# Optimization experiments

Measured on AMD Instinct MI355X. Metric: run time of the kernel, lower is better.

Reference implementation:

```python
import jax, jax.numpy as jnp
import numpy as np

B, C, H, W = 16, 256, 32, 32
AD, SC, R = 16, 32, 4


def _conv1x1(x, w, b):
    # x: [B,Cin,H,W], w: [Cout,Cin], b: [Cout]
    return jnp.einsum('oc,bchw->bohw', w, x) + b[None, :, None, None]


def setup_inputs() -> dict:
    key = jax.random.key(0)
    ks = jax.random.split(key, 12)
    p = lambda k, shape: (jax.random.normal(k, shape, dtype=jnp.float32) * 0.02)
    return {
        'x': jax.random.normal(ks[0], (B, C, H, W), dtype=jnp.float32),
        'fc1_w': p(ks[1], (C // R, C)), 'fc1_b': jnp.zeros((C // R,), jnp.float32),
        'fc2_w': p(ks[2], (C, C // R)), 'fc2_b': jnp.zeros((C,), jnp.float32),
        'qkv_w': p(ks[3], (AD * 2 + SC, SC)), 'qkv_b': jnp.zeros((AD * 2 + SC,), jnp.float32),
        'proj_w': p(ks[4], (SC, SC)), 'proj_b': jnp.zeros((SC,), jnp.float32),
        'ffn1_w': p(ks[5], (4 * C, C)), 'ffn1_b': jnp.zeros((4 * C,), jnp.float32),
        'ffn2_w': p(ks[6], (C, 4 * C)), 'ffn2_b': jnp.zeros((C,), jnp.float32),
    }


def reference(x, fc1_w, fc1_b, fc2_w, fc2_b, qkv_w, qkv_b, proj_w, proj_b,
              ffn1_w, ffn1_b, ffn2_w, ffn2_b):
    # --- DynamicChannelSelect: SE gate then channel split ---
    s = x.mean(axis=(2, 3), keepdims=True)                       # [B,C,1,1]
    s = jax.nn.relu(_conv1x1(s, fc1_w, fc1_b))
    s = jax.nn.sigmoid(_conv1x1(s, fc2_w, fc2_b))
    xg = x * s
    attn_part, non_attn_part = xg[:, :SC], xg[:, SC:]

    # --- SHSA: single-head self-attention on SC channels ---
    qkv = _conv1x1(attn_part, qkv_w, qkv_b)                      # [B,2*AD+SC,H,W]
    q = qkv[:, :AD].reshape(B, AD, H * W)
    k = qkv[:, AD:2 * AD].reshape(B, AD, H * W)
    v = qkv[:, 2 * AD:].reshape(B, SC, H * W)
    scale = AD ** -0.5
    attn = jax.nn.softmax(jnp.einsum('bcn,bcm->bnm', q, k) * scale, axis=-1)  # [B,N,N]
    out = jnp.einsum('bcm,bnm->bcn', v, attn).reshape(B, SC, H, W)
    attn_out = _conv1x1(out, proj_w, proj_b)

    # --- concat + 1x1-conv FFN ---
    y = jnp.concatenate([attn_out, non_attn_part], axis=1)       # [B,C,H,W]
    h = jax.nn.relu(_conv1x1(y, ffn1_w, ffn1_b))                 # [B,4C,H,W]
    return _conv1x1(h, ffn2_w, ffn2_b)                           # [B,C,H,W]
```

## Files before the change

kernel.cpp:

```cpp
#include <hip/hip_runtime.h>
#include <cstdint>
#include <cstddef>

#define BB 16
#define CC 256
#define NP 1024

typedef __attribute__((ext_vector_type(8))) short bf16x8;
typedef __attribute__((ext_vector_type(4))) float f32x4;
typedef unsigned short u16;

__device__ __forceinline__ u16 f2bf(float f) {
    union { float f; uint32_t u; } v; v.f = f;
    uint32_t u = v.u;
    return (u16)((u + 0x7FFFu + ((u >> 16) & 1u)) >> 16);
}

__global__ __launch_bounds__(256)
void se_mean_kernel(const float* __restrict__ x, float* __restrict__ s_mean) {
    int bc = blockIdx.x;
    const float* p = x + (size_t)bc * NP;
    int t = threadIdx.x;
    float4 v = *(const float4*)(p + t * 4);
    float s = (v.x + v.y) + (v.z + v.w);
#pragma unroll
    for (int off = 32; off; off >>= 1) s += __shfl_down(s, off, 64);
    __shared__ float red[4];
    if ((t & 63) == 0) red[t >> 6] = s;
    __syncthreads();
    if (t == 0) s_mean[bc] = (red[0] + red[1] + red[2] + red[3]) * (1.0f / NP);
}

__global__ __launch_bounds__(256)
void se_mlp_kernel(const float* __restrict__ s_mean,
                   const float* __restrict__ fc1_w, const float* __restrict__ fc1_b,
                   const float* __restrict__ fc2_w, const float* __restrict__ fc2_b,
                   float* __restrict__ sig) {
    int b = blockIdx.x;
    __shared__ float sm[CC];
    __shared__ float h1[64];
    int t = threadIdx.x;
    sm[t] = s_mean[b * CC + t];
    __syncthreads();
    if (t < 64) {
        float a = fc1_b[t];
        for (int c = 0; c < CC; ++c) a += fc1_w[t * CC + c] * sm[c];
        h1[t] = fmaxf(a, 0.f);
    }
    __syncthreads();
    float a = fc2_b[t];
#pragma unroll 8
    for (int c = 0; c < 64; ++c) a += fc2_w[t * 64 + c] * h1[c];
    sig[b * CC + t] = 1.f / (1.f + __expf(-a));
}

__global__ __launch_bounds__(256)
void scale_transpose_kernel(const float* __restrict__ x, const float* __restrict__ sig,
                            float* __restrict__ yg32, u16* __restrict__ ygt) {
    int nt = blockIdx.x, ct = blockIdx.y, b = blockIdx.z;
    __shared__ float tile[64][65];
    int t = threadIdx.x;
    const float* Xb = x + ((size_t)b * CC + ct * 64) * NP + nt * 64;
    float* ygb = yg32 + (size_t)b * 32 * NP + nt * 64;
#pragma unroll
    for (int p = 0; p < 4; ++p) {
        int e = t + p * 256;
        int c = e >> 4, n4 = (e & 15) * 4;
        float4 v = *(const float4*)&Xb[(size_t)c * NP + n4];
        float sc = sig[b * CC + ct * 64 + c];
        v.x *= sc; v.y *= sc; v.z *= sc; v.w *= sc;
        tile[c][n4] = v.x; tile[c][n4 + 1] = v.y; tile[c][n4 + 2] = v.z; tile[c][n4 + 3] = v.w;
        if (ct == 0 && c < 32) *(float4*)&ygb[(size_t)c * NP + n4] = v;
    }
    __syncthreads();
    u16* Yb = ygt + ((size_t)b * NP + nt * 64) * CC + ct * 64;
#pragma unroll
    for (int p = 0; p < 4; ++p) {
        int e = t + p * 256;
        int n = e >> 4, c4 = (e & 15) * 4;
        if (ct * 64 + c4 >= 32) {
            ushort4 o;
            o.x = f2bf(tile[c4][n]);     o.y = f2bf(tile[c4 + 1][n]);
            o.z = f2bf(tile[c4 + 2][n]); o.w = f2bf(tile[c4 + 3][n]);
            *(ushort4*)&Yb[(size_t)n * CC + c4] = o;
        }
    }
}

__global__ __launch_bounds__(256)
void qkv_kernel(const float* __restrict__ yg32,
                const float* __restrict__ W, const float* __restrict__ bias,
                u16* __restrict__ Qt, u16* __restrict__ Kt, u16* __restrict__ Vb) {
    int nt = blockIdx.x, b = blockIdx.y;
    const float* Xb = yg32 + (size_t)b * 32 * NP + nt * 64;
    __shared__ __align__(16) float xs[32][64];
    __shared__ float ws[64 * 32];
    __shared__ float bs[64];
    __shared__ float vtile[32][64];
    int t = threadIdx.x;
    for (int e = t * 4; e < 32 * 64; e += 1024) {
        int c = e >> 6, nn = e & 63;
        *(float4*)&xs[c][nn] = *(const float4*)&Xb[(size_t)c * NP + nn];
    }
    for (int e = t; e < 2048; e += 256) ws[e] = W[e];
    if (t < 64) bs[t] = bias[t];
    __syncthreads();
    int nn = t & 63, g = t >> 6;
    int n = nt * 64 + nn;
    float acc[16];
#pragma unroll
    for (int oc = 0; oc < 16; ++oc) {
        int o = g * 16 + oc;
        float a = bs[o];
#pragma unroll
        for (int c = 0; c < 32; ++c) a += ws[o * 32 + c] * xs[c][nn];
        acc[oc] = a;
    }
    if (g == 0) {
        u16* qr = Qt + ((size_t)b * NP + n) * 32;
        ushort4 z4; z4.x = 0; z4.y = 0; z4.z = 0; z4.w = 0;
#pragma unroll
        for (int j = 0; j < 16; j += 4) {
            ushort4 o4;
            o4.x = f2bf(acc[j] * 0.25f);     o4.y = f2bf(acc[j + 1] * 0.25f);
            o4.z = f2bf(acc[j + 2] * 0.25f); o4.w = f2bf(acc[j + 3] * 0.25f);
            *(ushort4*)&qr[j] = o4;
        }
        *(ushort4*)&qr[16] = z4; *(ushort4*)&qr[20] = z4;
        *(ushort4*)&qr[24] = z4; *(ushort4*)&qr[28] = z4;
    } else if (g == 1) {
        u16* kr = Kt + ((size_t)b * NP + n) * 32;
        ushort4 z4; z4.x = 0; z4.y = 0; z4.z = 0; z4.w = 0;
#pragma unroll
        for (int j = 0; j < 16; j += 4) {
            ushort4 k4;
            k4.x = f2bf(acc[j]);     k4.y = f2bf(acc[j + 1]);
            k4.z = f2bf(acc[j + 2]); k4.w = f2bf(acc[j + 3]);
            *(ushort4*)&kr[j] = k4;
        }
        *(ushort4*)&kr[16] = z4; *(ushort4*)&kr[20] = z4;
        *(ushort4*)&kr[24] = z4; *(ushort4*)&kr[28] = z4;
    } else {
#pragma unroll
        for (int oc = 0; oc < 16; ++oc) vtile[(g - 2) * 16 + oc][nn] = acc[oc];
    }
    __syncthreads();
    for (int e = t; e < 32 * 64; e += 256) {
        int c = e >> 6, nn2 = e & 63;
        Vb[(size_t)b * 32 * NP + (size_t)c * NP + nt * 64 + nn2] = f2bf(vtile[c][nn2]);
    }
}

__global__ __launch_bounds__(256)
void attn_mfma_kernel(const u16* __restrict__ Qt, const u16* __restrict__ Kt,
                      const u16* __restrict__ Vb,
                      const float* __restrict__ proj_w, const float* __restrict__ proj_b,
                      u16* __restrict__ ygt) {
    int b = blockIdx.x >> 4;
    int n0 = (blockIdx.x & 15) * 64;
    __shared__ __align__(16) u16 P_lds[4][16][40];
    __shared__ float al_lds[4][16];
    __shared__ float lv_lds[4][16];
    __shared__ float O_lds[4][16][33];
    __shared__ float pw_s[32][32];
    __shared__ float pb_s[32];
    int t = threadIdx.x;
    int w = t >> 6, lane = t & 63;
    int q = lane >> 4, idx = lane & 15;

    for (int e = t; e < 1024; e += 256) pw_s[e >> 5][e & 31] = proj_w[e];
    if (t < 32) pb_s[t] = proj_b[t];
    __syncthreads();

    const u16* Qb = Qt + (size_t)b * NP * 32;
    const u16* Kb = Kt + (size_t)b * NP * 32;
    const u16* Vp = Vb + (size_t)b * 32 * NP;

    int nrow = n0 + w * 16 + idx;
    bf16x8 aq = *(const bf16x8*)&Qb[(size_t)nrow * 32 + q * 8];

    f32x4 O0 = {0.f, 0.f, 0.f, 0.f}, O1 = {0.f, 0.f, 0.f, 0.f};
    float m_run[4] = {-1e30f, -1e30f, -1e30f, -1e30f};
    float l_run[4] = {0.f, 0.f, 0.f, 0.f};

    for (int m0 = 0; m0 < NP; m0 += 32) {
        bf16x8 bk0 = *(const bf16x8*)&Kb[(size_t)(m0 + idx) * 32 + q * 8];
        bf16x8 bk1 = *(const bf16x8*)&Kb[(size_t)(m0 + 16 + idx) * 32 + q * 8];
        bf16x8 va0 = *(const bf16x8*)&Vp[(size_t)idx * NP + m0 + q * 8];
        bf16x8 va1 = *(const bf16x8*)&Vp[(size_t)(16 + idx) * NP + m0 + q * 8];
        f32x4 z = {0.f, 0.f, 0.f, 0.f};
        f32x4 S0 = __builtin_amdgcn_mfma_f32_16x16x32_bf16(aq, bk0, z, 0, 0, 0);
        f32x4 S1 = __builtin_amdgcn_mfma_f32_16x16x32_bf16(aq, bk1, z, 0, 0, 0);
        float mx[4], p0[4], p1[4], alpha[4];
#pragma unroll
        for (int r = 0; r < 4; ++r) mx[r] = fmaxf(S0[r], S1[r]);
#pragma unroll
        for (int off = 1; off < 16; off <<= 1)
#pragma unroll
            for (int r = 0; r < 4; ++r) mx[r] = fmaxf(mx[r], __shfl_xor(mx[r], off, 64));
#pragma unroll
        for (int r = 0; r < 4; ++r) {
            float nm = fmaxf(m_run[r], mx[r]);
            alpha[r] = __expf(m_run[r] - nm);
            m_run[r] = nm;
            p0[r] = __expf(S0[r] - nm);
            p1[r] = __expf(S1[r] - nm);
        }
#pragma unroll
        for (int r = 0; r < 4; ++r) {
            float s = p0[r] + p1[r];
#pragma unroll
            for (int off = 1; off < 16; off <<= 1) s += __shfl_xor(s, off, 64);
            l_run[r] = l_run[r] * alpha[r] + s;
        }
#pragma unroll
        for (int r = 0; r < 4; ++r) {
            P_lds[w][q * 4 + r][idx]      = f2bf(p0[r]);
            P_lds[w][q * 4 + r][idx + 16] = f2bf(p1[r]);
        }
        if (idx == 0) {
#pragma unroll
            for (int r = 0; r < 4; ++r) al_lds[w][q * 4 + r] = alpha[r];
        }
        float an = al_lds[w][idx];
#pragma unroll
        for (int r = 0; r < 4; ++r) { O0[r] *= an; O1[r] *= an; }
        bf16x8 pf = *(const bf16x8*)&P_lds[w][idx][q * 8];
        O0 = __builtin_amdgcn_mfma_f32_16x16x32_bf16(va0, pf, O0, 0, 0, 0);
        O1 = __builtin_amdgcn_mfma_f32_16x16x32_bf16(va1, pf, O1, 0, 0, 0);
    }
    if (idx == 0) {
#pragma unroll
        for (int r = 0; r < 4; ++r) lv_lds[w][q * 4 + r] = l_run[r];
    }
    float linv = 1.0f / lv_lds[w][idx];
#pragma unroll
    for (int r = 0; r < 4; ++r) {
        O_lds[w][idx][q * 4 + r]      = O0[r] * linv;
        O_lds[w][idx][q * 4 + r + 16] = O1[r] * linv;
    }
    float o0[4], o1[4];
#pragma unroll
    for (int r = 0; r < 4; ++r) { o0[r] = pb_s[q * 4 + r]; o1[r] = pb_s[q * 4 + r + 16]; }
#pragma unroll
    for (int c = 0; c < 32; ++c) {
        float xv = O_lds[w][idx][c];
#pragma unroll
        for (int r = 0; r < 4; ++r) {
            o0[r] += pw_s[q * 4 + r][c] * xv;
            o1[r] += pw_s[q * 4 + r + 16][c] * xv;
        }
    }
    u16* yrow = ygt + ((size_t)b * NP + nrow) * CC;
    ushort4 w0, w1;
    w0.x = f2bf(o0[0]); w0.y = f2bf(o0[1]); w0.z = f2bf(o0[2]); w0.w = f2bf(o0[3]);
    w1.x = f2bf(o1[0]); w1.y = f2bf(o1[1]); w1.z = f2bf(o1[2]); w1.w = f2bf(o1[3]);
    *(ushort4*)&yrow[q * 4] = w0;
    *(ushort4*)&yrow[q * 4 + 16] = w1;
}

__global__ __launch_bounds__(256)
void convert_w_kernel(const float* __restrict__ w1, u16* __restrict__ d1,
                      const float* __restrict__ w2, u16* __restrict__ d2) {
    int blk = blockIdx.x;
    const float* src = (blk < 256) ? w1 : w2;
    u16* dst = (blk < 256) ? d1 : d2;
    int i = ((blk & 255) * 256 + threadIdx.x) * 4;
    float4 v = *(const float4*)(src + i);
    ushort4 o;
    o.x = f2bf(v.x); o.y = f2bf(v.y); o.z = f2bf(v.z); o.w = f2bf(v.w);
    *(ushort4*)(dst + i) = o;
}

template <int K, bool RELU, bool TRANS_OUT>
__global__ __launch_bounds__(256)
void mfma_gemm_kernel(const u16* __restrict__ A, const u16* __restrict__ Bt,
                      const float* __restrict__ bias, void* __restrict__ Yv, int M) {
    __shared__ __align__(16) u16 As[128][64];
    __shared__ __align__(16) u16 Bs[128][64];
    int mt = blockIdx.x, nt = blockIdx.y;
    const u16* Ab = A + (size_t)mt * 128 * K;
    const u16* Bb = Bt + (size_t)nt * 128 * K;
    int t = threadIdx.x;
    int w = t >> 6, lane = t & 63;
    int q = lane >> 4, idx = lane & 15;
    int wr = (w >> 1) * 64, wc = (w & 1) * 64;
    int srow = lane >> 3;
    int gch = (lane & 7) ^ srow;

    f32x4 acc[4][4];
#pragma unroll
    for (int i = 0; i < 4; ++i)
#pragma unroll
        for (int j = 0; j < 4; ++j) { f32x4 z = {0.f, 0.f, 0.f, 0.f}; acc[i][j] = z; }

    for (int k0 = 0; k0 < K; k0 += 64) {
        __syncthreads();
#pragma unroll
        for (int p = 0; p < 4; ++p) {
            int r = w * 32 + p * 8 + srow;
            __builtin_amdgcn_global_load_lds(
                (const __attribute__((address_space(1))) void*)(Ab + (size_t)r * K + k0 + gch * 8),
                (__attribute__((address_space(3))) void*)(&As[w * 32 + p * 8][0]),
                16, 0, 0);
        }
#pragma unroll
        for (int p = 0; p < 4; ++p) {
            int r = w * 32 + p * 8 + srow;
            __builtin_amdgcn_global_load_lds(
                (const __attribute__((address_space(1))) void*)(Bb + (size_t)r * K + k0 + gch * 8),
                (__attribute__((address_space(3))) void*)(&Bs[w * 32 + p * 8][0]),
                16, 0, 0);
        }
        __syncthreads();
#pragma unroll
        for (int h = 0; h < 2; ++h) {
            bf16x8 af[4], bfr[4];
#pragma unroll
            for (int i = 0; i < 4; ++i)
                af[i] = *(const bf16x8*)&As[wr + i * 16 + idx][(((q + 4 * h) ^ (idx & 7)) * 8)];
#pragma unroll
            for (int j = 0; j < 4; ++j)
                bfr[j] = *(const bf16x8*)&Bs[wc + j * 16 + idx][(((q + 4 * h) ^ (idx & 7)) * 8)];
#pragma unroll
            for (int i = 0; i < 4; ++i)
#pragma unroll
                for (int j = 0; j < 4; ++j)
                    acc[i][j] = __builtin_amdgcn_mfma_f32_16x16x32_bf16(af[i], bfr[j], acc[i][j], 0, 0, 0);
        }
    }

    if (TRANS_OUT) {
        u16* Y = (u16*)Yv;
#pragma unroll
        for (int i = 0; i < 4; ++i) {
            int m0 = mt * 128 + wr + i * 16 + q * 4;
            float b0 = bias[m0], b1 = bias[m0 + 1], b2 = bias[m0 + 2], b3 = bias[m0 + 3];
#pragma unroll
            for (int j = 0; j < 4; ++j) {
                int n = nt * 128 + wc + j * 16 + idx;
                f32x4 v = acc[i][j];
                float r0 = v.x + b0, r1 = v.y + b1, r2 = v.z + b2, r3 = v.w + b3;
                if (RELU) {
                    r0 = fmaxf(r0, 0.f); r1 = fmaxf(r1, 0.f);
                    r2 = fmaxf(r2, 0.f); r3 = fmaxf(r3, 0.f);
                }
                ushort4 o;
                o.x = f2bf(r0); o.y = f2bf(r1); o.z = f2bf(r2); o.w = f2bf(r3);
                *(ushort4*)&Y[(size_t)n * (size_t)M + m0] = o;
            }
        }
    } else {
        float* Y = (float*)Yv;
#pragma unroll
        for (int i = 0; i < 4; ++i) {
            int m0 = mt * 128 + wr + i * 16 + q * 4;
            float b0 = bias[m0], b1 = bias[m0 + 1], b2 = bias[m0 + 2], b3 = bias[m0 + 3];
#pragma unroll
            for (int j = 0; j < 4; ++j) {
                int ng = nt * 128 + wc + j * 16 + idx;
                int bb = ng >> 10, nn = ng & 1023;
                f32x4 v = acc[i][j];
                float* p = Y + ((size_t)bb * M + m0) * NP + nn;
                p[0]      = v.x + b0;
                p[NP]     = v.y + b1;
                p[2 * NP] = v.z + b2;
                p[3 * NP] = v.w + b3;
            }
        }
    }
}

extern "C" void kernel_launch(void* const* d_in, const int* in_sizes, int n_in,
                              void* d_out, int out_size, void* d_ws, size_t ws_size,
                              hipStream_t stream) {
    const float* x      = (const float*)d_in[0];
    const float* fc1_w  = (const float*)d_in[1];
    const float* fc1_b  = (const float*)d_in[2];
    const float* fc2_w  = (const float*)d_in[3];
    const float* fc2_b  = (const float*)d_in[4];
    const float* qkv_w  = (const float*)d_in[5];
    const float* qkv_b  = (const float*)d_in[6];
    const float* proj_w = (const float*)d_in[7];
    const float* proj_b = (const float*)d_in[8];
    const float* ffn1_w = (const float*)d_in[9];
    const float* ffn1_b = (const float*)d_in[10];
    const float* ffn2_w = (const float*)d_in[11];
    const float* ffn2_b = (const float*)d_in[12];
    float* out = (float*)d_out;

    u16* w1b = (u16*)d_ws;
    u16* w2b = w1b + 262144;
    u16* ygt = w2b + 262144;
    u16* ht  = ygt + (size_t)BB * NP * CC;
    float* sig  = (float*)ht;
    float* s_mean = sig + BB * CC;
    float* yg32 = s_mean + BB * CC;
    u16* Qt = (u16*)(yg32 + (size_t)BB * 32 * NP);
    u16* Kt = Qt + (size_t)BB * NP * 32;
    u16* Vb = Kt + (size_t)BB * NP * 32;

    se_mean_kernel<<<BB * CC, 256, 0, stream>>>(x, s_mean);
    convert_w_kernel<<<512, 256, 0, stream>>>(ffn1_w, w1b, ffn2_w, w2b);
    se_mlp_kernel<<<BB, 256, 0, stream>>>(s_mean, fc1_w, fc1_b, fc2_w, fc2_b, sig);
    scale_transpose_kernel<<<dim3(16, 4, BB), 256, 0, stream>>>(x, sig, yg32, ygt);
    qkv_kernel<<<dim3(16, BB), 256, 0, stream>>>(yg32, qkv_w, qkv_b, Qt, Kt, Vb);
    attn_mfma_kernel<<<BB * 16, 256, 0, stream>>>(Qt, Kt, Vb, proj_w, proj_b, ygt);

    mfma_gemm_kernel<256, true, true><<<dim3(8, 128), 256, 0, stream>>>(
        w1b, ygt, ffn1_b, (void*)ht, 1024);
    mfma_gemm_kernel<1024, false, false><<<dim3(2, 128), 256, 0, stream>>>(
        w2b, ht, ffn2_b, (void*)out, 256);
}
```

Before: 192.6 us.

## Fuse QKV into scale-transpose, split attention keys across waves, double-buffer GEMM

Folds the QKV 1x1 conv into the scale/transpose kernel using the already-scaled tile in shared memory, removing the fp32 staging buffer and one launch. The attention kernel now uses 512 threads, with two wave groups each covering half the keys and merging their softmax statistics in shared memory, to raise parallelism. The FFN GEMM double-buffers its LDS tiles so the next K-slice load overlaps the current MFMA work. The trade-offs are more shared memory per block and an extra merge step in attention.

Measured after the change: 181.7 us. 5.6% less time.

```diff
diff --git a/kernel.cpp b/kernel.cpp
--- a/kernel.cpp
+++ b/kernel.cpp
@@ -55,13 +55,21 @@
 }
 
 __global__ __launch_bounds__(256)
-void scale_transpose_kernel(const float* __restrict__ x, const float* __restrict__ sig,
-                            float* __restrict__ yg32, u16* __restrict__ ygt) {
+void scale_transpose_qkv_kernel(const float* __restrict__ x, const float* __restrict__ sig,
+                                const float* __restrict__ qW, const float* __restrict__ qB,
+                                u16* __restrict__ ygt, u16* __restrict__ Qt,
+                                u16* __restrict__ Kt, u16* __restrict__ Vb) {
     int nt = blockIdx.x, ct = blockIdx.y, b = blockIdx.z;
     __shared__ float tile[64][65];
+    __shared__ float ws[64 * 32];
+    __shared__ float bs[64];
+    __shared__ float vtile[32][64];
     int t = threadIdx.x;
     const float* Xb = x + ((size_t)b * CC + ct * 64) * NP + nt * 64;
-    float* ygb = yg32 + (size_t)b * 32 * NP + nt * 64;
+    if (ct == 0) {
+        for (int e = t; e < 2048; e += 256) ws[e] = qW[e];
+        if (t < 64) bs[t] = qB[t];
+    }
 #pragma unroll
     for (int p = 0; p < 4; ++p) {
         int e = t + p * 256;
@@ -70,7 +78,6 @@
         float sc = sig[b * CC + ct * 64 + c];
         v.x *= sc; v.y *= sc; v.z *= sc; v.w *= sc;
         tile[c][n4] = v.x; tile[c][n4 + 1] = v.y; tile[c][n4 + 2] = v.z; tile[c][n4 + 3] = v.w;
-        if (ct == 0 && c < 32) *(float4*)&ygb[(size_t)c * NP + n4] = v;
     }
     __syncthreads();
     u16* Yb = ygt + ((size_t)b * NP + nt * 64) * CC + ct * 64;
@@ -85,90 +92,74 @@
             *(ushort4*)&Yb[(size_t)n * CC + c4] = o;
         }
     }
-}
-
-__global__ __launch_bounds__(256)
-void qkv_kernel(const float* __restrict__ yg32,
-                const float* __restrict__ W, const float* __restrict__ bias,
-                u16* __restrict__ Qt, u16* __restrict__ Kt, u16* __restrict__ Vb) {
-    int nt = blockIdx.x, b = blockIdx.y;
-    const float* Xb = yg32 + (size_t)b * 32 * NP + nt * 64;
-    __shared__ __align__(16) float xs[32][64];
-    __shared__ float ws[64 * 32];
-    __shared__ float bs[64];
-    __shared__ float vtile[32][64];
-    int t = threadIdx.x;
-    for (int e = t * 4; e < 32 * 64; e += 1024) {
-        int c = e >> 6, nn = e & 63;
-        *(float4*)&xs[c][nn] = *(const float4*)&Xb[(size_t)c * NP + nn];
-    }
-    for (int e = t; e < 2048; e += 256) ws[e] = W[e];
-    if (t < 64) bs[t] = bias[t];
-    __syncthreads();
-    int nn = t & 63, g = t >> 6;
-    int n = nt * 64 + nn;
-    float acc[16];
-#pragma unroll
-    for (int oc = 0; oc < 16; ++oc) {
-        int o = g * 16 + oc;
-        float a = bs[o];
-#pragma unroll
-        for (int c = 0; c < 32; ++c) a += ws[o * 32 + c] * xs[c][nn];
-        acc[oc] = a;
-    }
-    if (g == 0) {
-        u16* qr = Qt + ((size_t)b * NP + n) * 32;
-        ushort4 z4; z4.x = 0; z4.y = 0; z4.z = 0; z4.w = 0;
-#pragma unroll
-        for (int j = 0; j < 16; j += 4) {
-            ushort4 o4;
-            o4.x = f2bf(acc[j] * 0.25f);     o4.y = f2bf(acc[j + 1] * 0.25f);
-            o4.z = f2bf(acc[j + 2] * 0.25f); o4.w = f2bf(acc[j + 3] * 0.25f);
-            *(ushort4*)&qr[j] = o4;
-        }
-        *(ushort4*)&qr[16] = z4; *(ushort4*)&qr[20] = z4;
-        *(ushort4*)&qr[24] = z4; *(ushort4*)&qr[28] = z4;
-    } else if (g == 1) {
-        u16* kr = Kt + ((size_t)b * NP + n) * 32;
-        ushort4 z4; z4.x = 0; z4.y = 0; z4.z = 0; z4.w = 0;
-#pragma unroll
-        for (int j = 0; j < 16; j += 4) {
-            ushort4 k4;
-            k4.x = f2bf(acc[j]);     k4.y = f2bf(acc[j + 1]);
-            k4.z = f2bf(acc[j + 2]); k4.w = f2bf(acc[j + 3]);
-            *(ushort4*)&kr[j] = k4;
-        }
-        *(ushort4*)&kr[16] = z4; *(ushort4*)&kr[20] = z4;
-        *(ushort4*)&kr[24] = z4; *(ushort4*)&kr[28] = z4;
-    } else {
-#pragma unroll
-        for (int oc = 0; oc < 16; ++oc) vtile[(g - 2) * 16 + oc][nn] = acc[oc];
-    }
-    __syncthreads();
-    for (int e = t; e < 32 * 64; e += 256) {
-        int c = e >> 6, nn2 = e & 63;
-        Vb[(size_t)b * 32 * NP + (size_t)c * NP + nt * 64 + nn2] = f2bf(vtile[c][nn2]);
-    }
-}
-
-__global__ __launch_bounds__(256)
+    if (ct == 0) {
+        int nn = t & 63, g = t >> 6;
+        int n = nt * 64 + nn;
+        float acc[16];
+#pragma unroll
+        for (int oc = 0; oc < 16; ++oc) {
+            int o = g * 16 + oc;
+            float a = bs[o];
+#pragma unroll
+            for (int c = 0; c < 32; ++c) a += ws[o * 32 + c] * tile[c][nn];
+            acc[oc] = a;
+        }
+        if (g == 0) {
+            u16* qr = Qt + ((size_t)b * NP + n) * 32;
+            ushort4 z4; z4.x = 0; z4.y = 0; z4.z = 0; z4.w = 0;
+#pragma unroll
+            for (int j = 0; j < 16; j += 4) {
+                ushort4 o4;
+                o4.x = f2bf(acc[j] * 0.25f);     o4.y = f2bf(acc[j + 1] * 0.25f);
+                o4.z = f2bf(acc[j + 2] * 0.25f); o4.w = f2bf(acc[j + 3] * 0.25f);
+                *(ushort4*)&qr[j] = o4;
+            }
+            *(ushort4*)&qr[16] = z4; *(ushort4*)&qr[20] = z4;
+            *(ushort4*)&qr[24] = z4; *(ushort4*)&qr[28] = z4;
+        } else if (g == 1) {
+            u16* kr = Kt + ((size_t)b * NP + n) * 32;
+            ushort4 z4; z4.x = 0; z4.y = 0; z4.z = 0; z4.w = 0;
+#pragma unroll
+            for (int j = 0; j < 16; j += 4) {
+                ushort4 k4;
+                k4.x = f2bf(acc[j]);     k4.y = f2bf(acc[j + 1]);
+                k4.z = f2bf(acc[j + 2]); k4.w = f2bf(acc[j + 3]);
+                *(ushort4*)&kr[j] = k4;
+            }
+            *(ushort4*)&kr[16] = z4; *(ushort4*)&kr[20] = z4;
+            *(ushort4*)&kr[24] = z4; *(ushort4*)&kr[28] = z4;
+        } else {
+#pragma unroll
+            for (int oc = 0; oc < 16; ++oc) vtile[(g - 2) * 16 + oc][nn] = acc[oc];
+        }
+        __syncthreads();
+        for (int e = t; e < 2048; e += 256) {
+            int c = e >> 6, nn2 = e & 63;
+            Vb[(size_t)b * 32 * NP + (size_t)c * NP + nt * 64 + nn2] = f2bf(vtile[c][nn2]);
+        }
+    }
+}
+
+__global__ __launch_bounds__(512)
 void attn_mfma_kernel(const u16* __restrict__ Qt, const u16* __restrict__ Kt,
                       const u16* __restrict__ Vb,
                       const float* __restrict__ proj_w, const float* __restrict__ proj_b,
                       u16* __restrict__ ygt) {
     int b = blockIdx.x >> 4;
     int n0 = (blockIdx.x & 15) * 64;
-    __shared__ __align__(16) u16 P_lds[4][16][40];
-    __shared__ float al_lds[4][16];
-    __shared__ float lv_lds[4][16];
-    __shared__ float O_lds[4][16][33];
+    __shared__ __align__(16) u16 P_lds[8][16][40];
+    __shared__ float al_lds[8][16];
+    __shared__ float sm_lds[8][16];
+    __shared__ float sl_lds[8][16];
+    __shared__ float O_lds[8][16][33];
     __shared__ float pw_s[32][32];
     __shared__ float pb_s[32];
     int t = threadIdx.x;
     int w = t >> 6, lane = t & 63;
     int q = lane >> 4, idx = lane & 15;
-
-    for (int e = t; e < 1024; e += 256) pw_s[e >> 5][e & 31] = proj_w[e];
+    int rg = w & 3, kh = w >> 2;
+
+    for (int e = t; e < 1024; e += 512) pw_s[e >> 5][e & 31] = proj_w[e];
     if (t < 32) pb_s[t] = proj_b[t];
     __syncthreads();
 
@@ -176,14 +167,15 @@
     const u16* Kb = Kt + (size_t)b * NP * 32;
     const u16* Vp = Vb + (size_t)b * 32 * NP;
 
-    int nrow = n0 + w * 16 + idx;
+    int nrow = n0 + rg * 16 + idx;
     bf16x8 aq = *(const bf16x8*)&Qb[(size_t)nrow * 32 + q * 8];
 
     f32x4 O0 = {0.f, 0.f, 0.f, 0.f}, O1 = {0.f, 0.f, 0.f, 0.f};
     float m_run[4] = {-1e30f, -1e30f, -1e30f, -1e30f};
     float l_run[4] = {0.f, 0.f, 0.f, 0.f};
 
-    for (int m0 = 0; m0 < NP; m0 += 32) {
+    int mbase = kh * 512;
+    for (int m0 = mbase; m0 < mbase + 512; m0 += 32) {
         bf16x8 bk0 = *(const bf16x8*)&Kb[(size_t)(m0 + idx) * 32 + q * 8];
         bf16x8 bk1 = *(const bf16x8*)&Kb[(size_t)(m0 + 16 + idx) * 32 + q * 8];
         bf16x8 va0 = *(const bf16x8*)&Vp[(size_t)idx * NP + m0 + q * 8];
@@ -231,32 +223,48 @@
     }
     if (idx == 0) {
 #pragma unroll
-        for (int r = 0; r < 4; ++r) lv_lds[w][q * 4 + r] = l_run[r];
-    }
-    float linv = 1.0f / lv_lds[w][idx];
+        for (int r = 0; r < 4; ++r) {
+            sm_lds[w][q * 4 + r] = m_run[r];
+            sl_lds[w][q * 4 + r] = l_run[r];
+        }
+    }
 #pragma unroll
     for (int r = 0; r < 4; ++r) {
-        O_lds[w][idx][q * 4 + r]      = O0[r] * linv;
-        O_lds[w][idx][q * 4 + r + 16] = O1[r] * linv;
-    }
-    float o0[4], o1[4];
-#pragma unroll
-    for (int r = 0; r < 4; ++r) { o0[r] = pb_s[q * 4 + r]; o1[r] = pb_s[q * 4 + r + 16]; }
-#pragma unroll
-    for (int c = 0; c < 32; ++c) {
-        float xv = O_lds[w][idx][c];
+        O_lds[w][idx][q * 4 + r]      = O0[r];
+        O_lds[w][idx][q * 4 + r + 16] = O1[r];
+    }
+    __syncthreads();
+    if (w < 4) {
+        float ma = sm_lds[w][idx], mb = sm_lds[w + 4][idx];
+        float la = sl_lds[w][idx], lb = sl_lds[w + 4][idx];
+        float gm = fmaxf(ma, mb);
+        float ea = __expf(ma - gm), eb = __expf(mb - gm);
+        float linv = 1.f / (la * ea + lb * eb);
 #pragma unroll
         for (int r = 0; r < 4; ++r) {
-            o0[r] += pw_s[q * 4 + r][c] * xv;
-            o1[r] += pw_s[q * 4 + r + 16][c] * xv;
-        }
-    }
-    u16* yrow = ygt + ((size_t)b * NP + nrow) * CC;
-    ushort4 w0, w1;
-    w0.x = f2bf(o0[0]); w0.y = f2bf(o0[1]); w0.z = f2bf(o0[2]); w0.w = f2bf(o0[3]);
-    w1.x = f2bf(o1[0]); w1.y = f2bf(o1[1]); w1.z = f2bf(o1[2]); w1.w = f2bf(o1[3]);
-    *(ushort4*)&yrow[q * 4] = w0;
-    *(ushort4*)&yrow[q * 4 + 16] = w1;
+            int c0 = q * 4 + r;
+            O_lds[w][idx][c0]      = (O_lds[w][idx][c0] * ea + O_lds[w + 4][idx][c0] * eb) * linv;
+            O_lds[w][idx][c0 + 16] = (O_lds[w][idx][c0 + 16] * ea + O_lds[w + 4][idx][c0 + 16] * eb) * linv;
+        }
+        float o0[4], o1[4];
+#pragma unroll
+        for (int r = 0; r < 4; ++r) { o0[r] = pb_s[q * 4 + r]; o1[r] = pb_s[q * 4 + r + 16]; }
+#pragma unroll
+        for (int c = 0; c < 32; ++c) {
+            float xv = O_lds[w][idx][c];
+#pragma unroll
+            for (int r = 0; r < 4; ++r) {
+                o0[r] += pw_s[q * 4 + r][c] * xv;
+                o1[r] += pw_s[q * 4 + r + 16][c] * xv;
+            }
+        }
+        u16* yrow = ygt + ((size_t)b * NP + n0 + w * 16 + idx) * CC;
+        ushort4 w0, w1;
+        w0.x = f2bf(o0[0]); w0.y = f2bf(o0[1]); w0.z = f2bf(o0[2]); w0.w = f2bf(o0[3]);
+        w1.x = f2bf(o1[0]); w1.y = f2bf(o1[1]); w1.z = f2bf(o1[2]); w1.w = f2bf(o1[3]);
+        *(ushort4*)&yrow[q * 4] = w0;
+        *(ushort4*)&yrow[q * 4 + 16] = w1;
+    }
 }
 
 __global__ __launch_bounds__(256)
@@ -276,8 +284,9 @@
 __global__ __launch_bounds__(256)
 void mfma_gemm_kernel(const u16* __restrict__ A, const u16* __restrict__ Bt,
                       const float* __restrict__ bias, void* __restrict__ Yv, int M) {
-    __shared__ __align__(16) u16 As[128][64];
-    __shared__ __align__(16) u16 Bs[128][64];
+    __shared__ __align__(16) u16 As[2][128][64];
+    __shared__ __align__(16) u16 Bs[2][128][64];
+    constexpr int NIT = K / 64;
     int mt = blockIdx.x, nt = blockIdx.y;
     const u16* Ab = A + (size_t)mt * 128 * K;
     const u16* Bb = Bt + (size_t)nt * 128 * K;
@@ -294,34 +303,40 @@
 #pragma unroll
         for (int j = 0; j < 4; ++j) { f32x4 z = {0.f, 0.f, 0.f, 0.f}; acc[i][j] = z; }
 
-    for (int k0 = 0; k0 < K; k0 += 64) {
+#define ISSUE_LOADS(buf, k0)                                                              \
+    {                                                                                     \
+        _Pragma("unroll")                                                                 \
+        for (int p = 0; p < 4; ++p) {                                                     \
+            int r = w * 32 + p * 8 + srow;                                                \
+            __builtin_amdgcn_global_load_lds(                                             \
+                (const __attribute__((address_space(1))) void*)(Ab + (size_t)r * K + (k0) + gch * 8), \
+                (__attribute__((address_space(3))) void*)(&As[buf][w * 32 + p * 8][0]),   \
+                16, 0, 0);                                                                \
+        }                                                                                 \
+        _Pragma("unroll")                                                                 \
+        for (int p = 0; p < 4; ++p) {                                                     \
+            int r = w * 32 + p * 8 + srow;                                                \
+            __builtin_amdgcn_global_load_lds(                                             \
+                (const __attribute__((address_space(1))) void*)(Bb + (size_t)r * K + (k0) + gch * 8), \
+                (__attribute__((address_space(3))) void*)(&Bs[buf][w * 32 + p * 8][0]),   \
+                16, 0, 0);                                                                \
+        }                                                                                 \
+    }
+
+    ISSUE_LOADS(0, 0)
+    for (int ki = 0; ki < NIT; ++ki) {
+        int cur = ki & 1;
         __syncthreads();
-#pragma unroll
-        for (int p = 0; p < 4; ++p) {
-            int r = w * 32 + p * 8 + srow;
-            __builtin_amdgcn_global_load_lds(
-                (const __attribute__((address_space(1))) void*)(Ab + (size_t)r * K + k0 + gch * 8),
-                (__attribute__((address_space(3))) void*)(&As[w * 32 + p * 8][0]),
-                16, 0, 0);
-        }
-#pragma unroll
-        for (int p = 0; p < 4; ++p) {
-            int r = w * 32 + p * 8 + srow;
-            __builtin_amdgcn_global_load_lds(
-                (const __attribute__((address_space(1))) void*)(Bb + (size_t)r * K + k0 + gch * 8),
-                (__attribute__((address_space(3))) void*)(&Bs[w * 32 + p * 8][0]),
-                16, 0, 0);
-        }
-        __syncthreads();
+        if (ki + 1 < NIT) ISSUE_LOADS(cur ^ 1, (ki + 1) * 64)
 #pragma unroll
         for (int h = 0; h < 2; ++h) {
             bf16x8 af[4], bfr[4];
 #pragma unroll
             for (int i = 0; i < 4; ++i)
-                af[i] = *(const bf16x8*)&As[wr + i * 16 + idx][(((q + 4 * h) ^ (idx & 7)) * 8)];
+                af[i] = *(const bf16x8*)&As[cur][wr + i * 16 + idx][(((q + 4 * h) ^ (idx & 7)) * 8)];
 #pragma unroll
             for (int j = 0; j < 4; ++j)
-                bfr[j] = *(const bf16x8*)&Bs[wc + j * 16 + idx][(((q + 4 * h) ^ (idx & 7)) * 8)];
+                bfr[j] = *(const bf16x8*)&Bs[cur][wc + j * 16 + idx][(((q + 4 * h) ^ (idx & 7)) * 8)];
 #pragma unroll
             for (int i = 0; i < 4; ++i)
 #pragma unroll
@@ -329,6 +344,7 @@
                     acc[i][j] = __builtin_amdgcn_mfma_f32_16x16x32_bf16(af[i], bfr[j], acc[i][j], 0, 0, 0);
         }
     }
+#undef ISSUE_LOADS
 
     if (TRANS_OUT) {
         u16* Y = (u16*)Yv;
@@ -393,19 +409,18 @@
     u16* w2b = w1b + 262144;
     u16* ygt = w2b + 262144;
     u16* ht  = ygt + (size_t)BB * NP * CC;
-    float* sig  = (float*)ht;
+    float* sig    = (float*)ht;
     float* s_mean = sig + BB * CC;
-    float* yg32 = s_mean + BB * CC;
-    u16* Qt = (u16*)(yg32 + (size_t)BB * 32 * NP);
+    u16* Qt = (u16*)(s_mean + BB * CC);
     u16* Kt = Qt + (size_t)BB * NP * 32;
     u16* Vb = Kt + (size_t)BB * NP * 32;
 
     se_mean_kernel<<<BB * CC, 256, 0, stream>>>(x, s_mean);
     convert_w_kernel<<<512, 256, 0, stream>>>(ffn1_w, w1b, ffn2_w, w2b);
     se_mlp_kernel<<<BB, 256, 0, stream>>>(s_mean, fc1_w, fc1_b, fc2_w, fc2_b, sig);
-    scale_transpose_kernel<<<dim3(16, 4, BB), 256, 0, stream>>>(x, sig, yg32, ygt);
-    qkv_kernel<<<dim3(16, BB), 256, 0, stream>>>(yg32, qkv_w, qkv_b, Qt, Kt, Vb);
-    attn_mfma_kernel<<<BB * 16, 256, 0, stream>>>(Qt, Kt, Vb, proj_w, proj_b, ygt);
+    scale_transpose_qkv_kernel<<<dim3(16, 4, BB), 256, 0, stream>>>(
+        x, sig, qkv_w, qkv_b, ygt, Qt, Kt, Vb);
+    attn_mfma_kernel<<<BB * 16, 512, 0, stream>>>(Qt, Kt, Vb, proj_w, proj_b, ygt);
 
     mfma_gemm_kernel<256, true, true><<<dim3(8, 128), 256, 0, stream>>>(
         w1b, ygt, ffn1_b, (void*)ht, 1024);
```
